# Optimization experiments

Measured on AMD Instinct MI355X. Metric: run time of the kernel, lower is better.

The kernel has to match this reference:

```python
import jax, jax.numpy as jnp
import numpy as np
from jax import lax

DT = 1.0 / 120.0
B, T = 4096, 128
TWO_PI = 2.0 * np.pi


def setup_inputs() -> dict:
    key = jax.random.key(0)
    k1, k2, k3, k4 = jax.random.split(key, 4)
    return {
        "params": jax.random.normal(k1, (4,), jnp.float32),
        "covariance_params": jax.random.normal(k2, (7,), jnp.float32),
        "init_states": jax.random.normal(k3, (B, 6), jnp.float32),
        "measurements": jax.random.normal(k4, (B, T, 3), jnp.float32),
    }


def _wrap(a):
    # wrap angle innovation to [-pi, pi]
    return a - TWO_PI * jnp.round(a / TWO_PI)


def _smooth_loss(params, covariance_params, init_state, z):
    # z: [T, 3] measurements of (x, y, theta)
    friction = (jnp.tanh(params[0]) + 1.0) * 0.01
    damping = (jnp.tanh(params[1]) + 1.0) * 0.01
    cp = jax.nn.sigmoid(covariance_params)
    R = jnp.diag(cp[:3])                                    # [3,3] meas noise
    Q = jnp.diag(cp[jnp.array([3, 3, 4, 4, 5, 6])])         # [6,6] proc noise
    I6 = jnp.eye(6, dtype=z.dtype)
    Hm = jnp.zeros((3, 6), z.dtype).at[0, 0].set(1.).at[1, 1].set(1.).at[2, 4].set(1.)
    P0 = 0.01 * I6

    def f_and_F(s):
        # free-sliding puck dynamics: [x, y, dx, dy, th, dth]
        x, y, dx, dy, th, dth = s
        ndx = dx - DT * (damping * dx + friction * jnp.tanh(100. * dx))
        ndy = dy - DT * (damping * dy + friction * jnp.tanh(100. * dy))
        ndth = dth * (1.0 - DT * damping)
        ns = jnp.stack([x + DT * dx, y + DT * dy, ndx, ndy, th + DT * dth, ndth])
        gx = 1.0 - DT * (damping + friction * 100. * (1. - jnp.tanh(100. * dx) ** 2))
        gy = 1.0 - DT * (damping + friction * 100. * (1. - jnp.tanh(100. * dy) ** 2))
        F = (I6.at[0, 2].set(DT).at[1, 3].set(DT).at[4, 5].set(DT)
               .at[2, 2].set(gx).at[3, 3].set(gy).at[5, 5].set(1.0 - DT * damping))
        return ns, F

    def ekf_step(carry, zt):
        s, P = carry
        sp, F = f_and_F(s)
        Pp = F @ P @ F.T + Q
        S = Hm @ Pp @ Hm.T + R
        innov = zt - Hm @ sp
        innov = innov.at[2].set(_wrap(innov[2]))
        K = jnp.linalg.solve(S, Hm @ Pp).T          # Pp H^T S^-1
        s_new = sp + K @ innov
        P_new = (I6 - K @ Hm) @ Pp
        return (s_new, P_new), (s_new, P_new, sp, Pp, F)

    _, (sf, Pf, sp, Pp, Fs) = lax.scan(ekf_step, (init_state, P0), z)

    # RTS backward pass
    def rts_step(carry, inp):
        s_next, P_next = carry
        s_f, P_f, sp_n, Pp_n, F_n = inp
        G = jnp.linalg.solve(Pp_n, F_n @ P_f).T     # P_f F^T Pp^{-1}
        s_s = s_f + G @ (s_next - sp_n)
        P_s = P_f + G @ (P_next - Pp_n) @ G.T
        return (s_s, P_s), (s_s, P_s)

    inp = (sf[:-1], Pf[:-1], sp[1:], Pp[1:], Fs[1:])
    _, (s_sm_head, P_sm_head) = lax.scan(rts_step, (sf[-1], Pf[-1]), inp, reverse=True)
    s_sm = jnp.concatenate([s_sm_head, sf[-1:]], 0)   # [T,6]
    P_sm = jnp.concatenate([P_sm_head, Pf[-1:]], 0)   # [T,6,6]

    # log-lik style loss vs measurements[2:] (as in compute_loss)
    zz, st, Pt = z[2:], s_sm[2:], P_sm[2:]
    Sv = jnp.einsum('ij,tjk,lk->til', Hm, Pt, Hm) + R  # [T-2,3,3] meas-space var
    innov_xy = zz[:, :2] - st[:, :2]
    a = zz[:, 2] - st[:, 4]
    a = jnp.where(a > 1.5 * np.pi, a - TWO_PI, a)
    a = jnp.where(a < -1.5 * np.pi, a + TWO_PI, a)
    innov = jnp.concatenate([innov_xy, a[:, None]], 1)
    sign, logdet = jnp.linalg.slogdet(Sv)
    return jnp.sum(sign * jnp.exp(logdet) + jnp.einsum('ti,tij,tj->t', innov, Sv, innov))


def reference(params, covariance_params, init_states, measurements):
    per_seg = jax.vmap(_smooth_loss, in_axes=(None, None, 0, 0))(
        params, covariance_params, init_states, measurements)
    return jnp.sum(per_seg)
```

## Files before the change

kernel.cpp:

```cpp
#include <hip/hip_runtime.h>
#include <cmath>


namespace {

constexpr int B = 4096;
constexpr int T = 128;
constexpr int SPB = 64;
constexpr int NBLK = B / SPB;
constexpr int NTH = 3 * SPB;
constexpr int NT = B * 3;
constexpr float DTc     = 1.0f / 120.0f;
constexpr float TWO_PIc = 6.28318530717958647692f;
constexpr float PI_1_5  = 4.71238898038468985769f;
constexpr float INV_2PI = 0.15915494309189533577f;

__device__ __forceinline__ float frcp(float x) { return __builtin_amdgcn_rcpf(x); }

__device__ __forceinline__ float fast_tanh(float x) {
  float e = __expf(2.0f * x);
  return 1.0f - 2.0f * frcp(e + 1.0f);
}
__device__ __forceinline__ float sigmoidf(float x) {
  return frcp(1.0f + __expf(-x));
}

__global__ __launch_bounds__(NTH, 1) void fused_kernel(
    const float* __restrict__ params, const float* __restrict__ covp,
    const float* __restrict__ init_states, const float* __restrict__ z,
    float4* __restrict__ hist4, float* __restrict__ hist1,
    float2* __restrict__ aq, float* __restrict__ out) {
  const int tid = threadIdx.x;
  const int f = tid >> 6;
  const int sb = tid & 63;
  const int blk = blockIdx.x;
  const int seq = blk * SPB + sb;
  const int gid = blk * NTH + tid;

  const float friction = (fast_tanh(params[0]) + 1.0f) * 0.01f;
  const float damping  = (fast_tanh(params[1]) + 1.0f) * 0.01f;
  float cp[7];
#pragma unroll
  for (int i = 0; i < 7; i++) cp[i] = sigmoidf(covp[i]);
  const float dcoef = 1.0f - DTc * damping;
  const bool isTH = (f == 2);
  const float q0 = isTH ? cp[5] : cp[3];
  const float q1 = isTH ? cp[6] : cp[4];
  const float r  = cp[f];

  const int pidx = (f == 0) ? 0 : (f == 1) ? 1 : 4;
  const int vidx = (f == 0) ? 2 : (f == 1) ? 3 : 5;
  float p = init_states[seq * 6 + pidx];
  float v = init_states[seq * 6 + vidx];
  float P00 = 0.01f, P01 = 0.0f, P11 = 0.01f;

  const float* __restrict__ zp = z + (size_t)seq * (T * 3) + f;

  float zb[8];
#pragma unroll
  for (int i = 0; i < 8; i++) zb[i] = zp[i * 3];

#pragma unroll 8
  for (int t = 0; t < T; t++) {
    const int sl = t & 7;
    const float zc = zb[sl];
    const int tf = (t + 8 < T) ? (t + 8) : (T - 1);
    zb[sl] = zp[tf * 3];

    float g, tv;
    if (!isTH) {
      const float th = fast_tanh(100.0f * v);
      tv = v - DTc * (damping * v + friction * th);
      g = 1.0f - DTc * (damping + 100.0f * friction * (1.0f - th * th));
    } else {
      tv = dcoef * v;
      g = dcoef;
    }
    const float tp = p + DTc * v;
    const float u = P01 + DTc * P11;
    const float Pp00 = P00 + DTc * P01 + DTc * u + q0;
    const float Pp01 = g * u;
    const float Pp11 = g * (g * P11) + q1;
    const float iS = frcp(Pp00 + r);
    const float K0 = Pp00 * iS;
    const float K1 = Pp01 * iS;
    float e = zc - tp;
    if (isTH) e = e - TWO_PIc * rintf(e * INV_2PI);
    p = tp + K0 * e;
    v = tv + K1 * e;
    const float om = 1.0f - K0;
    P00 = om * Pp00;
    P01 = om * Pp01;
    P11 = Pp11 - K1 * Pp01;

    hist4[(size_t)t * NT + gid] = make_float4(p, v, P00, P01);
    hist1[(size_t)t * NT + gid] = P11;
  }

  {
    const float zl = zp[(T - 1) * 3];
    float e = zl - p;
    if (isTH) {
      if (e >  PI_1_5) e -= TWO_PIc;
      if (e < -PI_1_5) e += TWO_PIc;
    }
    const float a = P00 + r;
    aq[(size_t)(T - 1) * NT + gid] = make_float2(a, a * e * e);
  }

  float sp_ = p, sv_ = v, Ps00 = P00, Ps01 = P01, Ps11 = P11;

  float4 h4b[8];
  float h1b[8], zbb[8];
#pragma unroll
  for (int i = 0; i < 8; i++) {
    const int n2 = 126 - i;
    h4b[i] = hist4[(size_t)n2 * NT + gid];
    h1b[i] = hist1[(size_t)n2 * NT + gid];
    zbb[i] = zp[n2 * 3];
  }

#pragma unroll 8
  for (int i = 0; i < 128; i++) {
    const int n = 126 - i;
    const int sl = i & 7;
    const float4 h4 = h4b[sl];
    const float h1 = h1b[sl];
    const float zn_ = zbb[sl];
    const int nf = (n >= 10) ? (n - 8) : 2;
    h4b[sl] = hist4[(size_t)nf * NT + gid];
    h1b[sl] = hist1[(size_t)nf * NT + gid];
    zbb[sl] = zp[nf * 3];

    const float fp = h4.x, fv = h4.y, f00 = h4.z, f01 = h4.w, f11 = h1;

    float g, tv;
    if (!isTH) {
      const float th = fast_tanh(100.0f * fv);
      tv = fv - DTc * (damping * fv + friction * th);
      g = 1.0f - DTc * (damping + 100.0f * friction * (1.0f - th * th));
    } else {
      tv = dcoef * fv;
      g = dcoef;
    }
    const float tp = fp + DTc * fv;
    const float u = f01 + DTc * f11;
    const float Pp00 = f00 + DTc * f01 + DTc * u + q0;
    const float Pp01 = g * u;
    const float Pp11 = g * (g * f11) + q1;

    const float idet = frcp(Pp00 * Pp11 - Pp01 * Pp01);
    const float W00 = f00, W01 = DTc * f00 + g * f01;
    const float W10 = f01, W11 = DTc * f01 + g * f11;
    const float G00 = (W00 * Pp11 - W01 * Pp01) * idet;
    const float G01 = (W01 * Pp00 - W00 * Pp01) * idet;
    const float G10 = (W10 * Pp11 - W11 * Pp01) * idet;
    const float G11 = (W11 * Pp00 - W10 * Pp01) * idet;

    const float ds0 = sp_ - tp, ds1 = sv_ - tv;
    const float np = fp + G00 * ds0 + G01 * ds1;
    const float nv = fv + G10 * ds0 + G11 * ds1;

    const float M00 = Ps00 - Pp00, M01 = Ps01 - Pp01, M11 = Ps11 - Pp11;
    const float GM00 = G00 * M00 + G01 * M01, GM01 = G00 * M01 + G01 * M11;
    const float GM10 = G10 * M00 + G11 * M01, GM11 = G10 * M01 + G11 * M11;
    Ps00 = f00 + GM00 * G00 + GM01 * G01;
    Ps01 = f01 + GM00 * G10 + GM01 * G11;
    Ps11 = f11 + GM10 * G10 + GM11 * G11;
    sp_ = np;
    sv_ = nv;

    if (n >= 2) {
      const float a = Ps00 + r;
      float e = zn_ - np;
      if (isTH) {
        if (e >  PI_1_5) e -= TWO_PIc;
        if (e < -PI_1_5) e += TWO_PIc;
      }
      aq[(size_t)n * NT + gid] = make_float2(a, a * e * e);
    }
  }

  __syncthreads();

  float part = 0.0f;
  const int base = blk * NTH;

  float2 b0[4], b1[4], b2[4];
#pragma unroll
  for (int k = 0; k < 4; k++) {
    const int pi = tid + k * NTH;
    const size_t o = (size_t)(2 + (pi >> 6)) * NT + base + (pi & 63);
    b0[k] = aq[o];
    b1[k] = aq[o + 64];
    b2[k] = aq[o + 128];
  }

#pragma unroll 4
  for (int k = 0; k < 44; k++) {
    const int sl = k & 3;
    const float2 x0 = b0[sl];
    const float2 x1 = b1[sl];
    const float2 x2 = b2[sl];
    const int kf = (k + 4 < 42) ? (k + 4) : 41;
    {
      const int pi = tid + kf * NTH;
      const size_t o = (size_t)(2 + (pi >> 6)) * NT + base + (pi & 63);
      b0[sl] = aq[o];
      b1[sl] = aq[o + 64];
      b2[sl] = aq[o + 128];
    }
    if (k < 42) part += x0.x * x1.x * x2.x + (x0.y + x1.y + x2.y);
  }

#pragma unroll
  for (int off = 32; off > 0; off >>= 1) part += __shfl_down(part, off);
  __shared__ float red[3];
  if ((tid & 63) == 0) red[tid >> 6] = part;
  __syncthreads();
  if (tid == 0) atomicAdd(out, red[0] + red[1] + red[2]);
}

}

extern "C" void kernel_launch(void* const* d_in, const int* in_sizes, int n_in,
                              void* d_out, int out_size, void* d_ws, size_t ws_size,
                              hipStream_t stream) {
  const float* params      = (const float*)d_in[0];
  const float* covp        = (const float*)d_in[1];
  const float* init_states = (const float*)d_in[2];
  const float* z           = (const float*)d_in[3];
  float* out = (float*)d_out;

  const size_t hist4B = (size_t)T * NT * sizeof(float4);
  const size_t hist1B = (size_t)T * NT * sizeof(float);
  const size_t aqB    = (size_t)T * NT * sizeof(float2);
  const size_t needBytes = hist4B + hist1B + aqB;

  hipMemsetAsync(d_out, 0, sizeof(float), stream);

  if (ws_size >= needBytes) {
    float4* hist4 = (float4*)d_ws;
    float*  hist1 = (float*)((char*)d_ws + hist4B);
    float2* aqp   = (float2*)((char*)d_ws + hist4B + hist1B);
    fused_kernel<<<NBLK, NTH, 0, stream>>>(params, covp, init_states, z,
                                           hist4, hist1, aqp, out);
  }
}
```

Measured before the change: 123.0 us.

## Split fused kernel into one-wave chain kernel and separate determinant reduction

Each 64-lane block now processes one state component for 64 sequences, giving 192 single-wave blocks where there were 64 three-wave blocks, so the serial chains spread across more CUs. The quadratic term is accumulated in registers during the backward pass, and only the diagonal variance is stored. A second kernel reads the three variances per timestep and sums their products. The aim is better CU coverage for the latency-bound recurrences and a smaller aq store. The cost is an extra launch and more atomics on the output.

Measured after the change: 123.0 us. No clear change (-0.0%).

```diff
diff --git a/kernel.cpp b/kernel.cpp
--- a/kernel.cpp
+++ b/kernel.cpp
@@ -6,10 +6,9 @@
 
 constexpr int B = 4096;
 constexpr int T = 128;
-constexpr int SPB = 64;
-constexpr int NBLK = B / SPB;
-constexpr int NTH = 3 * SPB;
 constexpr int NT = B * 3;
+constexpr int NBLK1 = 192;
+constexpr int TRIPLES = 126 * B;
 constexpr float DTc     = 1.0f / 120.0f;
 constexpr float TWO_PIc = 6.28318530717958647692f;
 constexpr float PI_1_5  = 4.71238898038468985769f;
@@ -25,17 +24,17 @@
   return frcp(1.0f + __expf(-x));
 }
 
-__global__ __launch_bounds__(NTH, 1) void fused_kernel(
+__global__ __launch_bounds__(64, 1) void chains_kernel(
     const float* __restrict__ params, const float* __restrict__ covp,
     const float* __restrict__ init_states, const float* __restrict__ z,
     float4* __restrict__ hist4, float* __restrict__ hist1,
-    float2* __restrict__ aq, float* __restrict__ out) {
-  const int tid = threadIdx.x;
-  const int f = tid >> 6;
-  const int sb = tid & 63;
+    float* __restrict__ aqA, float* __restrict__ out) {
+  const int lane = threadIdx.x;
   const int blk = blockIdx.x;
-  const int seq = blk * SPB + sb;
-  const int gid = blk * NTH + tid;
+  const int f = blk >> 6;
+  const int g = blk & 63;
+  const int seq = g * 64 + lane;
+  const int fi = f * B + seq;
 
   const float friction = (fast_tanh(params[0]) + 1.0f) * 0.01f;
   const float damping  = (fast_tanh(params[1]) + 1.0f) * 0.01f;
@@ -56,6 +55,8 @@
 
   const float* __restrict__ zp = z + (size_t)seq * (T * 3) + f;
 
+  float qacc = 0.0f;
+
   float zb[8];
 #pragma unroll
   for (int i = 0; i < 8; i++) zb[i] = zp[i * 3];
@@ -67,20 +68,20 @@
     const int tf = (t + 8 < T) ? (t + 8) : (T - 1);
     zb[sl] = zp[tf * 3];
 
-    float g, tv;
+    float gg, tv;
     if (!isTH) {
       const float th = fast_tanh(100.0f * v);
       tv = v - DTc * (damping * v + friction * th);
-      g = 1.0f - DTc * (damping + 100.0f * friction * (1.0f - th * th));
+      gg = 1.0f - DTc * (damping + 100.0f * friction * (1.0f - th * th));
     } else {
       tv = dcoef * v;
-      g = dcoef;
+      gg = dcoef;
     }
     const float tp = p + DTc * v;
     const float u = P01 + DTc * P11;
     const float Pp00 = P00 + DTc * P01 + DTc * u + q0;
-    const float Pp01 = g * u;
-    const float Pp11 = g * (g * P11) + q1;
+    const float Pp01 = gg * u;
+    const float Pp11 = gg * (gg * P11) + q1;
     const float iS = frcp(Pp00 + r);
     const float K0 = Pp00 * iS;
     const float K1 = Pp01 * iS;
@@ -93,8 +94,8 @@
     P01 = om * Pp01;
     P11 = Pp11 - K1 * Pp01;
 
-    hist4[(size_t)t * NT + gid] = make_float4(p, v, P00, P01);
-    hist1[(size_t)t * NT + gid] = P11;
+    hist4[(size_t)t * NT + fi] = make_float4(p, v, P00, P01);
+    hist1[(size_t)t * NT + fi] = P11;
   }
 
   {
@@ -105,7 +106,8 @@
       if (e < -PI_1_5) e += TWO_PIc;
     }
     const float a = P00 + r;
-    aq[(size_t)(T - 1) * NT + gid] = make_float2(a, a * e * e);
+    qacc += a * e * e;
+    aqA[(size_t)((T - 1) * 3 + f) * B + seq] = a;
   }
 
   float sp_ = p, sv_ = v, Ps00 = P00, Ps01 = P01, Ps11 = P11;
@@ -115,8 +117,8 @@
 #pragma unroll
   for (int i = 0; i < 8; i++) {
     const int n2 = 126 - i;
-    h4b[i] = hist4[(size_t)n2 * NT + gid];
-    h1b[i] = hist1[(size_t)n2 * NT + gid];
+    h4b[i] = hist4[(size_t)n2 * NT + fi];
+    h1b[i] = hist1[(size_t)n2 * NT + fi];
     zbb[i] = zp[n2 * 3];
   }
 
@@ -128,30 +130,30 @@
     const float h1 = h1b[sl];
     const float zn_ = zbb[sl];
     const int nf = (n >= 10) ? (n - 8) : 2;
-    h4b[sl] = hist4[(size_t)nf * NT + gid];
-    h1b[sl] = hist1[(size_t)nf * NT + gid];
+    h4b[sl] = hist4[(size_t)nf * NT + fi];
+    h1b[sl] = hist1[(size_t)nf * NT + fi];
     zbb[sl] = zp[nf * 3];
 
     const float fp = h4.x, fv = h4.y, f00 = h4.z, f01 = h4.w, f11 = h1;
 
-    float g, tv;
+    float gg, tv;
     if (!isTH) {
       const float th = fast_tanh(100.0f * fv);
       tv = fv - DTc * (damping * fv + friction * th);
-      g = 1.0f - DTc * (damping + 100.0f * friction * (1.0f - th * th));
+      gg = 1.0f - DTc * (damping + 100.0f * friction * (1.0f - th * th));
     } else {
       tv = dcoef * fv;
-      g = dcoef;
+      gg = dcoef;
     }
     const float tp = fp + DTc * fv;
     const float u = f01 + DTc * f11;
     const float Pp00 = f00 + DTc * f01 + DTc * u + q0;
-    const float Pp01 = g * u;
-    const float Pp11 = g * (g * f11) + q1;
+    const float Pp01 = gg * u;
+    const float Pp11 = gg * (gg * f11) + q1;
 
     const float idet = frcp(Pp00 * Pp11 - Pp01 * Pp01);
-    const float W00 = f00, W01 = DTc * f00 + g * f01;
-    const float W10 = f01, W11 = DTc * f01 + g * f11;
+    const float W00 = f00, W01 = DTc * f00 + gg * f01;
+    const float W10 = f01, W11 = DTc * f01 + gg * f11;
     const float G00 = (W00 * Pp11 - W01 * Pp01) * idet;
     const float G01 = (W01 * Pp00 - W00 * Pp01) * idet;
     const float G10 = (W10 * Pp11 - W11 * Pp01) * idet;
@@ -177,48 +179,35 @@
         if (e >  PI_1_5) e -= TWO_PIc;
         if (e < -PI_1_5) e += TWO_PIc;
       }
-      aq[(size_t)n * NT + gid] = make_float2(a, a * e * e);
-    }
-  }
-
+      qacc += a * e * e;
+      aqA[(size_t)(n * 3 + f) * B + seq] = a;
+    }
+  }
+
+#pragma unroll
+  for (int off = 32; off > 0; off >>= 1) qacc += __shfl_down(qacc, off);
+  if (lane == 0) atomicAdd(out, qacc);
+}
+
+__global__ __launch_bounds__(256, 4) void det_kernel(
+    const float* __restrict__ aqA, float* __restrict__ out) {
+  const int tid0 = blockIdx.x * 256 + threadIdx.x;
+  const int stride = gridDim.x * 256;
+  float part = 0.0f;
+  for (int idx = tid0; idx < TRIPLES; idx += stride) {
+    const int n2 = 2 + (idx >> 12);
+    const int seq = idx & (B - 1);
+    const float a0 = aqA[(size_t)(n2 * 3 + 0) * B + seq];
+    const float a1 = aqA[(size_t)(n2 * 3 + 1) * B + seq];
+    const float a2 = aqA[(size_t)(n2 * 3 + 2) * B + seq];
+    part += a0 * a1 * a2;
+  }
+#pragma unroll
+  for (int off = 32; off > 0; off >>= 1) part += __shfl_down(part, off);
+  __shared__ float red[4];
+  if ((threadIdx.x & 63) == 0) red[threadIdx.x >> 6] = part;
   __syncthreads();
-
-  float part = 0.0f;
-  const int base = blk * NTH;
-
-  float2 b0[4], b1[4], b2[4];
-#pragma unroll
-  for (int k = 0; k < 4; k++) {
-    const int pi = tid + k * NTH;
-    const size_t o = (size_t)(2 + (pi >> 6)) * NT + base + (pi & 63);
-    b0[k] = aq[o];
-    b1[k] = aq[o + 64];
-    b2[k] = aq[o + 128];
-  }
-
-#pragma unroll 4
-  for (int k = 0; k < 44; k++) {
-    const int sl = k & 3;
-    const float2 x0 = b0[sl];
-    const float2 x1 = b1[sl];
-    const float2 x2 = b2[sl];
-    const int kf = (k + 4 < 42) ? (k + 4) : 41;
-    {
-      const int pi = tid + kf * NTH;
-      const size_t o = (size_t)(2 + (pi >> 6)) * NT + base + (pi & 63);
-      b0[sl] = aq[o];
-      b1[sl] = aq[o + 64];
-      b2[sl] = aq[o + 128];
-    }
-    if (k < 42) part += x0.x * x1.x * x2.x + (x0.y + x1.y + x2.y);
-  }
-
-#pragma unroll
-  for (int off = 32; off > 0; off >>= 1) part += __shfl_down(part, off);
-  __shared__ float red[3];
-  if ((tid & 63) == 0) red[tid >> 6] = part;
-  __syncthreads();
-  if (tid == 0) atomicAdd(out, red[0] + red[1] + red[2]);
+  if (threadIdx.x == 0) atomicAdd(out, red[0] + red[1] + red[2] + red[3]);
 }
 
 }
@@ -234,7 +223,7 @@
 
   const size_t hist4B = (size_t)T * NT * sizeof(float4);
   const size_t hist1B = (size_t)T * NT * sizeof(float);
-  const size_t aqB    = (size_t)T * NT * sizeof(float2);
+  const size_t aqB    = (size_t)T * 3 * B * sizeof(float);
   const size_t needBytes = hist4B + hist1B + aqB;
 
   hipMemsetAsync(d_out, 0, sizeof(float), stream);
@@ -242,8 +231,9 @@
   if (ws_size >= needBytes) {
     float4* hist4 = (float4*)d_ws;
     float*  hist1 = (float*)((char*)d_ws + hist4B);
-    float2* aqp   = (float2*)((char*)d_ws + hist4B + hist1B);
-    fused_kernel<<<NBLK, NTH, 0, stream>>>(params, covp, init_states, z,
-                                           hist4, hist1, aqp, out);
-  }
-}
+    float*  aqA   = (float*)((char*)d_ws + hist4B + hist1B);
+    chains_kernel<<<NBLK1, 64, 0, stream>>>(params, covp, init_states, z,
+                                            hist4, hist1, aqA, out);
+    det_kernel<<<504, 256, 0, stream>>>(aqA, out);
+  }
+}
```
